# Optimization experiments

Measured on AMD Instinct MI355X. Metric: run time of the kernel, lower is better.

The kernel has to match this reference:

```python
import jax, jax.numpy as jnp
import numpy as np

DIM, N_HEAD, DK, DV = 1024, 16, 64, 64
B, S = 1, 4096


def setup_inputs() -> dict:
    key = jax.random.key(0)
    ks = jax.random.split(key, 9)
    sd = 0.02
    return {
        "x": jax.random.normal(ks[0], (B, S, DIM), dtype=jnp.float32),
        "Wq": jax.random.normal(ks[1], (DIM, N_HEAD * DK), dtype=jnp.float32) * sd,
        "bq": jnp.zeros((N_HEAD * DK,), dtype=jnp.float32),
        "Wk": jax.random.normal(ks[2], (DIM, N_HEAD * DK), dtype=jnp.float32) * sd,
        "bk": jnp.zeros((N_HEAD * DK,), dtype=jnp.float32),
        "Wv": jax.random.normal(ks[3], (DIM, N_HEAD * DV), dtype=jnp.float32) * sd,
        "bv": jnp.zeros((N_HEAD * DV,), dtype=jnp.float32),
        "Wo": jax.random.normal(ks[4], (N_HEAD * DV, DIM), dtype=jnp.float32) * sd,
        "bo": jnp.zeros((DIM,), dtype=jnp.float32),
    }


def reference(x, Wq, bq, Wk, bk, Wv, bv, Wo, bo):
    b, s, _ = x.shape
    scale = DK ** (-0.5)
    # projections -> [b, h, s, d]
    q = (x @ Wq + bq).reshape(b, s, N_HEAD, DK).transpose(0, 2, 1, 3)
    k = (x @ Wk + bk).reshape(b, s, N_HEAD, DK).transpose(0, 2, 1, 3)
    v = (x @ Wv + bv).reshape(b, s, N_HEAD, DV).transpose(0, 2, 1, 3)
    attn = jnp.einsum("bhqd,bhkd->bhqk", q, k) * scale  # [b,h,s,s]
    attn = jax.nn.softmax(attn, axis=-1)
    out = jnp.einsum("bhqk,bhkd->bhqd", attn, v)  # [b,h,s,dv]
    out = out.transpose(0, 2, 1, 3).reshape(b, s, N_HEAD * DV)
    return out @ Wo + bo
```

## Files before the change

kernel.cpp:

```cpp
#include <hip/hip_runtime.h>
#include <hip/hip_bf16.h>
#include <hip/hip_fp16.h>

#define SEQ 4096
#define DIM 1024
#define NH 16
#define NT (SEQ / 64)

typedef __attribute__((ext_vector_type(4))) float f32x4;
typedef __attribute__((ext_vector_type(8))) _Float16 half8;
typedef __attribute__((ext_vector_type(4))) _Float16 half4;
typedef __attribute__((ext_vector_type(2))) unsigned uint2v;

#if __has_builtin(__builtin_amdgcn_exp2f)
#define EXP2(x) __builtin_amdgcn_exp2f(x)
#else
#define EXP2(x) exp2f(x)
#endif

#define SMC 0.18033688f


__global__ __launch_bounds__(256) void conv_x(const float* __restrict__ x,
                                              _Float16* __restrict__ xh, int n) {
  int i = (blockIdx.x * 256 + threadIdx.x) * 4;
  if (i >= n) return;
  float4 v = *reinterpret_cast<const float4*>(x + i);
  half4 h;
  h[0] = (_Float16)v.x; h[1] = (_Float16)v.y;
  h[2] = (_Float16)v.z; h[3] = (_Float16)v.w;
  *reinterpret_cast<half4*>(xh + i) = h;
}

__global__ __launch_bounds__(256) void conv_wT4(const float* __restrict__ W0,
                                                const float* __restrict__ W1,
                                                const float* __restrict__ W2,
                                                const float* __restrict__ W3,
                                                _Float16* __restrict__ T0,
                                                _Float16* __restrict__ T1,
                                                _Float16* __restrict__ T2,
                                                _Float16* __restrict__ T3) {
  const float* W = blockIdx.z == 0 ? W0 : blockIdx.z == 1 ? W1 : blockIdx.z == 2 ? W2 : W3;
  _Float16* Wt = blockIdx.z == 0 ? T0 : blockIdx.z == 1 ? T1 : blockIdx.z == 2 ? T2 : T3;
  __shared__ float t[32][33];
  int bx = blockIdx.x * 32;
  int by = blockIdx.y * 32;
  int tx = threadIdx.x & 31, ty = threadIdx.x >> 5;
#pragma unroll
  for (int i = 0; i < 4; i++)
    t[ty + i * 8][tx] = W[(by + ty + i * 8) * DIM + bx + tx];
  __syncthreads();
#pragma unroll
  for (int i = 0; i < 4; i++)
    Wt[(bx + ty + i * 8) * DIM + by + tx] = (_Float16)t[tx][ty + i * 8];
}

template <int MODE>
__device__ __forceinline__ void gemm_body(const _Float16* __restrict__ A,
                                          const _Float16* __restrict__ Bt,
                                          const float* __restrict__ bias,
                                          void* __restrict__ outp,
                                          int M, int N, int Kd, int bmb, int bnb) {
  __shared__ __align__(16) _Float16 As[64][72];
  __shared__ __align__(16) _Float16 Bs[128][72];
  const int tid = threadIdx.x, lane = tid & 63, w = tid >> 6;
  const int bm = bmb * 64, bn = bnb * 128;
  const int l15 = lane & 15, g = lane >> 4, kb = g * 8;
  const int sra = tid >> 2, sca = (tid & 3) * 16;
  const int srb = tid >> 1, scb = (tid & 1) * 32;
  f32x4 acc[4][2] = {};

  uint4 ar0, ar1, br0, br1, br2, br3;
  auto LOADT = [&](int k0) {
    const _Float16* ap = A + (size_t)(bm + sra) * Kd + k0 + sca;
    ar0 = *reinterpret_cast<const uint4*>(ap);
    ar1 = *reinterpret_cast<const uint4*>(ap + 8);
    const _Float16* bp = Bt + (size_t)(bn + srb) * Kd + k0 + scb;
    br0 = *reinterpret_cast<const uint4*>(bp);
    br1 = *reinterpret_cast<const uint4*>(bp + 8);
    br2 = *reinterpret_cast<const uint4*>(bp + 16);
    br3 = *reinterpret_cast<const uint4*>(bp + 24);
  };

  LOADT(0);
  for (int k0 = 0; k0 < Kd; k0 += 64) {
    __syncthreads();
    *reinterpret_cast<uint4*>(&As[sra][sca]) = ar0;
    *reinterpret_cast<uint4*>(&As[sra][sca + 8]) = ar1;
    *reinterpret_cast<uint4*>(&Bs[srb][scb]) = br0;
    *reinterpret_cast<uint4*>(&Bs[srb][scb + 8]) = br1;
    *reinterpret_cast<uint4*>(&Bs[srb][scb + 16]) = br2;
    *reinterpret_cast<uint4*>(&Bs[srb][scb + 24]) = br3;
    __syncthreads();
    if (k0 + 64 < Kd) LOADT(k0 + 64);
#pragma unroll
    for (int kk = 0; kk < 64; kk += 32) {
      half8 af[4], bf[2];
#pragma unroll
      for (int i = 0; i < 4; i++)
        af[i] = *reinterpret_cast<const half8*>(&As[i * 16 + l15][kk + kb]);
#pragma unroll
      for (int j = 0; j < 2; j++)
        bf[j] = *reinterpret_cast<const half8*>(&Bs[w * 32 + j * 16 + l15][kk + kb]);
      __builtin_amdgcn_s_setprio(1);
#pragma unroll
      for (int i = 0; i < 4; i++)
#pragma unroll
        for (int j = 0; j < 2; j++)
          acc[i][j] = __builtin_amdgcn_mfma_f32_16x16x32_f16(af[i], bf[j], acc[i][j], 0, 0, 0);
      __builtin_amdgcn_s_setprio(0);
    }
  }

#pragma unroll
  for (int i = 0; i < 4; i++)
#pragma unroll
    for (int j = 0; j < 2; j++) {
      const int row0 = bm + i * 16 + g * 4;
      const int col = bn + w * 32 + j * 16 + l15;
      if (MODE == 2) {
        half4 hv;
#pragma unroll
        for (int r = 0; r < 4; r++) hv[r] = (_Float16)(acc[i][j][r] + bias[col]);
        *reinterpret_cast<half4*>(&((_Float16*)outp)[(size_t)col * M + row0]) = hv;
      } else {
#pragma unroll
        for (int r = 0; r < 4; r++) {
          float vv = acc[i][j][r] + bias[col];
          if (MODE == 0) {
            _Float16* O = (_Float16*)outp;
            O[(((col >> 6) * SEQ) + row0 + r) * 64 + (col & 63)] = (_Float16)vv;
          } else {
            float* O = (float*)outp;
            O[(size_t)(row0 + r) * N + col] = vv;
          }
        }
      }
    }
}

__global__ __launch_bounds__(256) void gemm_qkv(const _Float16* __restrict__ A,
                                                const _Float16* __restrict__ WqT,
                                                const _Float16* __restrict__ WkT,
                                                const _Float16* __restrict__ WvT,
                                                const float* __restrict__ bq,
                                                const float* __restrict__ bk,
                                                const float* __restrict__ bv,
                                                _Float16* __restrict__ Qd,
                                                _Float16* __restrict__ Kd,
                                                _Float16* __restrict__ Vd) {
  if (blockIdx.z == 0)
    gemm_body<0>(A, WqT, bq, (void*)Qd, SEQ, DIM, DIM, blockIdx.x, blockIdx.y);
  else if (blockIdx.z == 1)
    gemm_body<0>(A, WkT, bk, (void*)Kd, SEQ, DIM, DIM, blockIdx.x, blockIdx.y);
  else
    gemm_body<2>(A, WvT, bv, (void*)Vd, SEQ, DIM, DIM, blockIdx.x, blockIdx.y);
}

__global__ __launch_bounds__(256) void gemm_out(const _Float16* __restrict__ A,
                                                const _Float16* __restrict__ Bt,
                                                const float* __restrict__ bias,
                                                float* __restrict__ out) {
  gemm_body<1>(A, Bt, bias, (void*)out, SEQ, DIM, DIM, blockIdx.x, blockIdx.y);
}

__global__ __launch_bounds__(256) void attn_fwd(const _Float16* __restrict__ Q,
                                                const _Float16* __restrict__ Kh,
                                                const _Float16* __restrict__ Vt_g,
                                                _Float16* __restrict__ Og) {
  __shared__ __align__(16) _Float16 Ks[2][64][72];
  __shared__ __align__(16) _Float16 Vs[2][64][72];
  const int h = blockIdx.y;
  const int q0 = blockIdx.x * 128;
  const int tid = threadIdx.x, lane = tid & 63, w = tid >> 6;
  const int l15 = lane & 15, g = lane >> 4, kb = g * 8;

  const int qrow = q0 + w * 32 + l15;
  const _Float16* qp = Q + ((size_t)h * SEQ + qrow) * 64;
  half8 qf[2][2];
  qf[0][0] = *reinterpret_cast<const half8*>(qp + kb);
  qf[0][1] = *reinterpret_cast<const half8*>(qp + 32 + kb);
  qf[1][0] = *reinterpret_cast<const half8*>(qp + 16 * 64 + kb);
  qf[1][1] = *reinterpret_cast<const half8*>(qp + 16 * 64 + 32 + kb);

  f32x4 o[2][4] = {};
  float m[2] = {-1e30f, -1e30f};
  float lsum[2] = {0.f, 0.f};
  float negmC[2] = {1e30f, 1e30f};

  const int srow = tid >> 3, sc8 = (tid & 7) * 8;
  const _Float16* kbase = Kh + (size_t)h * SEQ * 64;
  const _Float16* vbase = Vt_g + (size_t)h * 64 * SEQ;

  uint4 kr0, kr1, vr0, vr1;
  auto LOADKV = [&](int kt2) {
    const _Float16* kp = kbase + (size_t)(kt2 * 64 + srow) * 64 + sc8;
    kr0 = *reinterpret_cast<const uint4*>(kp);
    kr1 = *reinterpret_cast<const uint4*>(kp + 32 * 64);
    const _Float16* vp = vbase + (size_t)srow * SEQ + kt2 * 64 + sc8;
    vr0 = *reinterpret_cast<const uint4*>(vp);
    vr1 = *reinterpret_cast<const uint4*>(vp + 32 * SEQ);
  };
  auto STAGE = [&](int buf) {
    *reinterpret_cast<uint4*>(&Ks[buf][srow][sc8]) = kr0;
    *reinterpret_cast<uint4*>(&Ks[buf][srow + 32][sc8]) = kr1;
    *reinterpret_cast<uint4*>(&Vs[buf][srow][sc8]) = vr0;
    *reinterpret_cast<uint4*>(&Vs[buf][srow + 32][sc8]) = vr1;
  };

  LOADKV(0);
  STAGE(0);
  __syncthreads();
  int cur = 0;

  for (int kt = 0; kt < NT; ++kt) {
    const bool more = (kt + 1 < NT);
    if (more) LOADKV(kt + 1);

    f32x4 sf[2][4] = {};
    __builtin_amdgcn_s_setprio(1);
#pragma unroll
    for (int f = 0; f < 4; f++) {
      half8 kf0 = *reinterpret_cast<const half8*>(&Ks[cur][f * 16 + l15][kb]);
      half8 kf1 = *reinterpret_cast<const half8*>(&Ks[cur][f * 16 + l15][32 + kb]);
      sf[0][f] = __builtin_amdgcn_mfma_f32_16x16x32_f16(kf0, qf[0][0], sf[0][f], 0, 0, 0);
      sf[0][f] = __builtin_amdgcn_mfma_f32_16x16x32_f16(kf1, qf[0][1], sf[0][f], 0, 0, 0);
      sf[1][f] = __builtin_amdgcn_mfma_f32_16x16x32_f16(kf0, qf[1][0], sf[1][f], 0, 0, 0);
      sf[1][f] = __builtin_amdgcn_mfma_f32_16x16x32_f16(kf1, qf[1][1], sf[1][f], 0, 0, 0);
    }
    __builtin_amdgcn_s_setprio(0);

    half4 pb[2][4];
#pragma unroll
    for (int s = 0; s < 2; s++) {
      float pm = fmaxf(fmaxf(fmaxf(sf[s][0][0], sf[s][0][1]), fmaxf(sf[s][0][2], sf[s][0][3])),
                       fmaxf(fmaxf(sf[s][1][0], sf[s][1][1]), fmaxf(sf[s][1][2], sf[s][1][3])));
      pm = fmaxf(pm, fmaxf(fmaxf(fmaxf(sf[s][2][0], sf[s][2][1]), fmaxf(sf[s][2][2], sf[s][2][3])),
                           fmaxf(fmaxf(sf[s][3][0], sf[s][3][1]), fmaxf(sf[s][3][2], sf[s][3][3]))));
      if (__any(pm > m[s] + 64.f)) {
        pm = fmaxf(pm, __shfl_xor(pm, 16, 64));
        pm = fmaxf(pm, __shfl_xor(pm, 32, 64));
        float mn = fmaxf(m[s], pm);
        float al = EXP2((m[s] - mn) * SMC);
        m[s] = mn;
        negmC[s] = -mn * SMC;
        lsum[s] *= al;
#pragma unroll
        for (int f = 0; f < 4; f++) o[s][f] *= al;
      }
#pragma unroll
      for (int f = 0; f < 4; f++) {
        float p0 = EXP2(fmaf(sf[s][f][0], SMC, negmC[s]));
        float p1 = EXP2(fmaf(sf[s][f][1], SMC, negmC[s]));
        float p2 = EXP2(fmaf(sf[s][f][2], SMC, negmC[s]));
        float p3 = EXP2(fmaf(sf[s][f][3], SMC, negmC[s]));
        lsum[s] += (p0 + p1) + (p2 + p3);
        auto h01 = __builtin_amdgcn_cvt_pkrtz(p0, p1);
        auto h23 = __builtin_amdgcn_cvt_pkrtz(p2, p3);
        uint2v uu = {__builtin_bit_cast(unsigned, h01), __builtin_bit_cast(unsigned, h23)};
        pb[s][f] = __builtin_bit_cast(half4, uu);
      }
    }

    __builtin_amdgcn_s_setprio(1);
#pragma unroll
    for (int fv = 0; fv < 4; fv++) {
#pragma unroll
      for (int fk = 0; fk < 4; fk++) {
        half4 va = *reinterpret_cast<const half4*>(&Vs[cur][fv * 16 + l15][fk * 16 + g * 4]);
        o[0][fv] = __builtin_amdgcn_mfma_f32_16x16x16f16(va, pb[0][fk], o[0][fv], 0, 0, 0);
        o[1][fv] = __builtin_amdgcn_mfma_f32_16x16x16f16(va, pb[1][fk], o[1][fv], 0, 0, 0);
      }
    }
    __builtin_amdgcn_s_setprio(0);

    if (more) STAGE(cur ^ 1);
    __syncthreads();
    cur ^= 1;
  }

#pragma unroll
  for (int s = 0; s < 2; s++) {
    float ls = lsum[s];
    ls += __shfl_xor(ls, 16, 64);
    ls += __shfl_xor(ls, 32, 64);
    float rinv = 1.f / ls;
#pragma unroll
    for (int f = 0; f < 4; f++) {
      half4 hv;
#pragma unroll
      for (int r = 0; r < 4; r++) hv[r] = (_Float16)(o[s][f][r] * rinv);
      *reinterpret_cast<half4*>(
          &Og[(size_t)(qrow + 16 * s) * DIM + h * 64 + f * 16 + g * 4]) = hv;
    }
  }
}


extern "C" void kernel_launch(void* const* d_in, const int* in_sizes, int n_in,
                              void* d_out, int out_size, void* d_ws, size_t ws_size,
                              hipStream_t stream) {
  const float* x  = (const float*)d_in[0];
  const float* Wq = (const float*)d_in[1];
  const float* bq = (const float*)d_in[2];
  const float* Wk = (const float*)d_in[3];
  const float* bk = (const float*)d_in[4];
  const float* Wv = (const float*)d_in[5];
  const float* bv = (const float*)d_in[6];
  const float* Wo = (const float*)d_in[7];
  const float* bo = (const float*)d_in[8];

  char* ws = (char*)d_ws;
  _Float16* xh  = (_Float16*)ws;
  _Float16* WqT = (_Float16*)(ws + (size_t)SEQ * DIM * 2);
  _Float16* WkT = WqT + DIM * DIM;
  _Float16* WvT = WkT + DIM * DIM;
  _Float16* WoT = WvT + DIM * DIM;
  _Float16* Qd  = WoT + DIM * DIM;
  _Float16* Kd  = Qd + (size_t)SEQ * DIM;
  _Float16* Vd  = Kd + (size_t)SEQ * DIM;
  _Float16* Od  = Vd + (size_t)SEQ * DIM;

  conv_x<<<(SEQ * DIM) / 1024, 256, 0, stream>>>(x, xh, SEQ * DIM);
  conv_wT4<<<dim3(32, 32, 4), 256, 0, stream>>>(Wq, Wk, Wv, Wo, WqT, WkT, WvT, WoT);

  gemm_qkv<<<dim3(SEQ / 64, DIM / 128, 3), 256, 0, stream>>>(
      xh, WqT, WkT, WvT, bq, bk, bv, Qd, Kd, Vd);

  attn_fwd<<<dim3(SEQ / 128, NH), 256, 0, stream>>>(Qd, Kd, Vd, Od);

  gemm_out<<<dim3(SEQ / 64, DIM / 128), 256, 0, stream>>>(Od, WoT, bo, (float*)d_out);
}
```

Measured before the change: 188.6 us.

## Software-pipeline QK^T of next tile with softmax/PV of current tile, triple-buffer K/V

Restructures the attention loop so the QK^T MFMAs for tile t+1 are issued before the softmax and PV work of tile t, letting the exp/VALU work overlap matrix-core work. K/V shared buffers grow from two to three, with global loads issued two tiles ahead. This hides MFMA and LDS latency behind softmax at the cost of more LDS, which may reduce occupancy, and a second set of score registers, which raises register pressure.

```diff
diff --git a/kernel.cpp b/kernel.cpp
--- a/kernel.cpp
+++ b/kernel.cpp
@@ -168,8 +168,8 @@
                                                 const _Float16* __restrict__ Kh,
                                                 const _Float16* __restrict__ Vt_g,
                                                 _Float16* __restrict__ Og) {
-  __shared__ __align__(16) _Float16 Ks[2][64][72];
-  __shared__ __align__(16) _Float16 Vs[2][64][72];
+  __shared__ __align__(16) _Float16 Ks[3][64][72];
+  __shared__ __align__(16) _Float16 Vs[3][64][72];
   const int h = blockIdx.y;
   const int q0 = blockIdx.x * 128;
   const int tid = threadIdx.x, lane = tid & 63, w = tid >> 6;
@@ -208,35 +208,37 @@
     *reinterpret_cast<uint4*>(&Vs[buf][srow + 32][sc8]) = vr1;
   };
 
-  LOADKV(0);
-  STAGE(0);
-  __syncthreads();
-  int cur = 0;
-
-  for (int kt = 0; kt < NT; ++kt) {
-    const bool more = (kt + 1 < NT);
-    if (more) LOADKV(kt + 1);
-
-    f32x4 sf[2][4] = {};
+  auto QK = [&](int tile, f32x4 (&sf)[2][4]) {
+    const int b = tile % 3;
     __builtin_amdgcn_s_setprio(1);
 #pragma unroll
     for (int f = 0; f < 4; f++) {
-      half8 kf0 = *reinterpret_cast<const half8*>(&Ks[cur][f * 16 + l15][kb]);
-      half8 kf1 = *reinterpret_cast<const half8*>(&Ks[cur][f * 16 + l15][32 + kb]);
+      half8 kf0 = *reinterpret_cast<const half8*>(&Ks[b][f * 16 + l15][kb]);
+      half8 kf1 = *reinterpret_cast<const half8*>(&Ks[b][f * 16 + l15][32 + kb]);
       sf[0][f] = __builtin_amdgcn_mfma_f32_16x16x32_f16(kf0, qf[0][0], sf[0][f], 0, 0, 0);
       sf[0][f] = __builtin_amdgcn_mfma_f32_16x16x32_f16(kf1, qf[0][1], sf[0][f], 0, 0, 0);
       sf[1][f] = __builtin_amdgcn_mfma_f32_16x16x32_f16(kf0, qf[1][0], sf[1][f], 0, 0, 0);
       sf[1][f] = __builtin_amdgcn_mfma_f32_16x16x32_f16(kf1, qf[1][1], sf[1][f], 0, 0, 0);
     }
     __builtin_amdgcn_s_setprio(0);
+  };
+
+  auto ITER = [&](int t, f32x4 (&scur)[2][4], f32x4 (&snext)[2][4]) {
+    if (t + 1 < NT) {
+#pragma unroll
+      for (int s = 0; s < 2; s++)
+#pragma unroll
+        for (int f = 0; f < 4; f++) snext[s][f] = (f32x4){0.f, 0.f, 0.f, 0.f};
+      QK(t + 1, snext);
+    }
 
     half4 pb[2][4];
 #pragma unroll
     for (int s = 0; s < 2; s++) {
-      float pm = fmaxf(fmaxf(fmaxf(sf[s][0][0], sf[s][0][1]), fmaxf(sf[s][0][2], sf[s][0][3])),
-                       fmaxf(fmaxf(sf[s][1][0], sf[s][1][1]), fmaxf(sf[s][1][2], sf[s][1][3])));
-      pm = fmaxf(pm, fmaxf(fmaxf(fmaxf(sf[s][2][0], sf[s][2][1]), fmaxf(sf[s][2][2], sf[s][2][3])),
-                           fmaxf(fmaxf(sf[s][3][0], sf[s][3][1]), fmaxf(sf[s][3][2], sf[s][3][3]))));
+      float pm = fmaxf(fmaxf(fmaxf(scur[s][0][0], scur[s][0][1]), fmaxf(scur[s][0][2], scur[s][0][3])),
+                       fmaxf(fmaxf(scur[s][1][0], scur[s][1][1]), fmaxf(scur[s][1][2], scur[s][1][3])));
+      pm = fmaxf(pm, fmaxf(fmaxf(fmaxf(scur[s][2][0], scur[s][2][1]), fmaxf(scur[s][2][2], scur[s][2][3])),
+                           fmaxf(fmaxf(scur[s][3][0], scur[s][3][1]), fmaxf(scur[s][3][2], scur[s][3][3]))));
       if (__any(pm > m[s] + 64.f)) {
         pm = fmaxf(pm, __shfl_xor(pm, 16, 64));
         pm = fmaxf(pm, __shfl_xor(pm, 32, 64));
@@ -250,10 +252,10 @@
       }
 #pragma unroll
       for (int f = 0; f < 4; f++) {
-        float p0 = EXP2(fmaf(sf[s][f][0], SMC, negmC[s]));
-        float p1 = EXP2(fmaf(sf[s][f][1], SMC, negmC[s]));
-        float p2 = EXP2(fmaf(sf[s][f][2], SMC, negmC[s]));
-        float p3 = EXP2(fmaf(sf[s][f][3], SMC, negmC[s]));
+        float p0 = EXP2(fmaf(scur[s][f][0], SMC, negmC[s]));
+        float p1 = EXP2(fmaf(scur[s][f][1], SMC, negmC[s]));
+        float p2 = EXP2(fmaf(scur[s][f][2], SMC, negmC[s]));
+        float p3 = EXP2(fmaf(scur[s][f][3], SMC, negmC[s]));
         lsum[s] += (p0 + p1) + (p2 + p3);
         auto h01 = __builtin_amdgcn_cvt_pkrtz(p0, p1);
         auto h23 = __builtin_amdgcn_cvt_pkrtz(p2, p3);
@@ -262,21 +264,34 @@
       }
     }
 
+    const int bv = t % 3;
     __builtin_amdgcn_s_setprio(1);
 #pragma unroll
     for (int fv = 0; fv < 4; fv++) {
 #pragma unroll
       for (int fk = 0; fk < 4; fk++) {
-        half4 va = *reinterpret_cast<const half4*>(&Vs[cur][fv * 16 + l15][fk * 16 + g * 4]);
+        half4 va = *reinterpret_cast<const half4*>(&Vs[bv][fv * 16 + l15][fk * 16 + g * 4]);
         o[0][fv] = __builtin_amdgcn_mfma_f32_16x16x16f16(va, pb[0][fk], o[0][fv], 0, 0, 0);
         o[1][fv] = __builtin_amdgcn_mfma_f32_16x16x16f16(va, pb[1][fk], o[1][fv], 0, 0, 0);
       }
     }
     __builtin_amdgcn_s_setprio(0);
 
-    if (more) STAGE(cur ^ 1);
+    if (t + 2 < NT) STAGE((t + 2) % 3);
+    if (t + 3 < NT) LOADKV(t + 3);
     __syncthreads();
-    cur ^= 1;
+  };
+
+  LOADKV(0); STAGE(0);
+  LOADKV(1); STAGE(1);
+  LOADKV(2);
+  __syncthreads();
+
+  f32x4 sfA[2][4] = {}, sfB[2][4] = {};
+  QK(0, sfA);
+  for (int t = 0; t < NT; t += 2) {
+    ITER(t, sfA, sfB);
+    ITER(t + 1, sfB, sfA);
   }
 
 #pragma unroll
```

After: 185.8 us. No clear change (-1.4%).
